# Kernel optimization log

Measured on AMD Instinct MI355X. Metric: run time of the kernel, lower is better.

Reference implementation:

```python
import jax, jax.numpy as jnp
import numpy as np

BITS = 4
GROUP_SIZE = 128
IN_FEATURES = 4096
OUT_FEATURES = 14336
M = 256  # rows of x; >= kernel_switch_threshold so torch takes the dequant+matmul path


def setup_inputs() -> dict:
    key = jax.random.key(0)
    k1, k2, k3, k4 = jax.random.split(key, 4)
    x = jax.random.normal(k1, (M, IN_FEATURES), dtype=jnp.float16)
    # packed int4 weights: in_features//32*bits rows of int32
    qweight = jax.random.randint(
        k2, (IN_FEATURES // 32 * BITS, OUT_FEATURES), 0, 2**31 - 1, dtype=jnp.int32
    )
    n_groups = IN_FEATURES // GROUP_SIZE
    scales = jax.random.uniform(k3, (n_groups, OUT_FEATURES), dtype=jnp.float32) * 0.01 + 0.001
    # note: module stores zeros as scale*zero product (see pack()); any float works
    zeros = jax.random.uniform(k4, (n_groups, OUT_FEATURES), dtype=jnp.float32) * 0.05
    return {"x": x, "qweight": qweight, "scales": scales, "zeros": zeros}


def reference(x, qweight, scales, zeros):
    # Unpack 8 int4 values from each int32 (little-endian nibbles), matching
    # torch: (qweight[:,None,:] >> wf) & 0xF with wf = [0,4,...,28].
    shifts = jnp.arange(0, 32, BITS, dtype=jnp.int32)          # [8]
    w = (qweight[:, None, :] >> shifts[None, :, None]) & (2**BITS - 1)  # [K/8, 8, N]
    w = w.reshape(-1, GROUP_SIZE, qweight.shape[1])             # [n_groups, group, N]
    s = scales.astype(jnp.float16)[:, None, :]                  # [n_groups, 1, N]
    z = zeros.astype(jnp.float16)[:, None, :]
    # group-wise asymmetric dequant: scale * q - (scale*zero)
    w = (s * w.astype(jnp.float16) - z).reshape(-1, qweight.shape[1])  # [K, N]
    out = jnp.matmul(x, w)                                      # [M, N] fp16
    return out.astype(x.dtype)
```

## Files before the change

### kernel.cpp

```cpp
#include <hip/hip_runtime.h>
#include <hip/hip_fp16.h>

typedef unsigned int u32;
typedef unsigned short u16;
typedef __attribute__((ext_vector_type(8))) _Float16 f16x8;
typedef __attribute__((ext_vector_type(4))) float f32x4;
typedef __attribute__((ext_vector_type(4))) u32 u32x4;

#define K_DIM 4096
#define N_DIM 14336
#define BM 64
#define BN 128
#define BK 64
#define NITER 32
#define NBLK 448
#define LDA 72

union U4F8 { u32x4 u; f16x8 v; };

__device__ __forceinline__ f16x8 dq8(u32 q, __half2 s2, __half2 d2, __half2 z2) {
  U4F8 r;
  const u32 x0 = ( q        & 0x000F000Fu) | 0x64006400u;
  const u32 x1 = ((q >> 4)  & 0x000F000Fu) | 0x64006400u;
  const u32 x2 = ((q >> 8)  & 0x000F000Fu) | 0x64006400u;
  const u32 x3 = ((q >> 12) & 0x000F000Fu) | 0x64006400u;
  r.u.x = __builtin_bit_cast(u32, __hsub2(__hfma2(__builtin_bit_cast(__half2, x0), s2, d2), z2));
  r.u.y = __builtin_bit_cast(u32, __hsub2(__hfma2(__builtin_bit_cast(__half2, x1), s2, d2), z2));
  r.u.z = __builtin_bit_cast(u32, __hsub2(__hfma2(__builtin_bit_cast(__half2, x2), s2, d2), z2));
  r.u.w = __builtin_bit_cast(u32, __hsub2(__hfma2(__builtin_bit_cast(__half2, x3), s2, d2), z2));
  return r.v;
}

__device__ __forceinline__ u32 pkrtz(float a, float b) {
  return __builtin_bit_cast(u32, __builtin_amdgcn_cvt_pkrtz(a, b));
}

__global__ __launch_bounds__(512, 4) void kivi_gemm(
    const float* __restrict__ X,
    const int* __restrict__ QW,
    const float* __restrict__ S,
    const float* __restrict__ Z,
    float* __restrict__ O)
{
  __shared__ __align__(16) u16 As[2][2][BM][LDA];

  const int tid  = threadIdx.x;
  const int lane = tid & 63;
  const int w    = tid >> 6;
  const int ws   = w >> 2;
  const int wl   = w & 3;
  const int stid = tid & 255;

  const int b  = blockIdx.x;
  const int L  = (b & 7) * 56 + (b >> 3);
  const int m0 = (L & 3) * BM;
  const int n0 = (L >> 2) * BN;

  const int wm = wl >> 1, wn = wl & 1;
  const int mb = wm * 32, nb = wn * 64;
  const int fr = lane & 15, fq = lane >> 4;
  const int cb = n0 + nb + fr;

  const int arow = stid >> 2;
  const int acol = (stid & 3) * 16;

  f32x4 acc[2][4];
#pragma unroll
  for (int mi = 0; mi < 2; ++mi)
#pragma unroll
    for (int ni = 0; ni < 4; ++ni)
      acc[mi][ni] = (f32x4){0.f, 0.f, 0.f, 0.f};

  f32x4 aReg[4];
  u32 qReg[2][4];
  float sv[4], zv[4];

  auto loadAx = [&](int t) {
    const float* p = X + (size_t)(m0 + arow) * K_DIM + t * BK + acol;
    aReg[0] = *(const f32x4*)(p);
    aReg[1] = *(const f32x4*)(p + 4);
    aReg[2] = *(const f32x4*)(p + 8);
    aReg[3] = *(const f32x4*)(p + 12);
  };
  auto writeAx = [&](int buf) {
#pragma unroll
    for (int c = 0; c < 2; ++c) {
      u32x4 pk;
      pk.x = pkrtz(aReg[c * 2][0], aReg[c * 2 + 1][0]);
      pk.y = pkrtz(aReg[c * 2][1], aReg[c * 2 + 1][1]);
      pk.z = pkrtz(aReg[c * 2][2], aReg[c * 2 + 1][2]);
      pk.w = pkrtz(aReg[c * 2][3], aReg[c * 2 + 1][3]);
      *(u32x4*)&As[ws][buf][arow][acol + c * 8] = pk;
    }
  };
  auto loadBq = [&](int t, int g) {
    const size_t rbase = (size_t)(t * 8 + fq) * N_DIM + cb;
#pragma unroll
    for (int ks = 0; ks < 2; ++ks)
#pragma unroll
      for (int ni = 0; ni < 4; ++ni)
        qReg[ks][ni] = *(const u32*)(QW + rbase + (size_t)ks * 4 * N_DIM + ni * 16);
#pragma unroll
    for (int ni = 0; ni < 4; ++ni) {
      sv[ni] = S[(size_t)g * N_DIM + cb + ni * 16];
      zv[ni] = Z[(size_t)g * N_DIM + cb + ni * 16];
    }
  };

  loadAx(ws);
  loadBq(ws, 0);
  writeAx(0);
  __syncthreads();

  const __half hneg1024 = __float2half(-1024.f);

  for (int i = 0; i < NITER; ++i) {
    const int t   = 2 * i + ws;
    const int cur = i & 1;
    const bool pf = (i + 1 < NITER);

    if (pf) loadAx(t + 2);

    __half2 s2[4], d2[4], z2[4];
#pragma unroll
    for (int ni = 0; ni < 4; ++ni) {
      const __half sh = __float2half(sv[ni]);
      const __half zh = __float2half(zv[ni]);
      const __half dh = __hmul(sh, hneg1024);
      s2[ni] = __halves2half2(sh, sh);
      d2[ni] = __halves2half2(dh, dh);
      z2[ni] = __halves2half2(zh, zh);
    }

#pragma unroll
    for (int ks = 0; ks < 2; ++ks) {
      f16x8 af[2], bf[4];
#pragma unroll
      for (int mi = 0; mi < 2; ++mi)
        af[mi] = *(const f16x8*)&As[ws][cur][mb + mi * 16 + fr][ks * 32 + fq * 8];
#pragma unroll
      for (int ni = 0; ni < 4; ++ni)
        bf[ni] = dq8(qReg[ks][ni], s2[ni], d2[ni], z2[ni]);
#pragma unroll
      for (int mi = 0; mi < 2; ++mi)
#pragma unroll
        for (int ni = 0; ni < 4; ++ni)
          acc[mi][ni] = __builtin_amdgcn_mfma_f32_16x16x32_f16(
              af[mi], bf[ni], acc[mi][ni], 0, 0, 0);
    }

    if (pf) {
      writeAx(cur ^ 1);
      loadBq(t + 2, i + 1);
    }
    __syncthreads();
  }

  float (*Lr)[132] = reinterpret_cast<float(*)[132]>(&As[0][0][0][0]);
  if (ws == 1) {
#pragma unroll
    for (int mi = 0; mi < 2; ++mi)
#pragma unroll
      for (int ni = 0; ni < 4; ++ni)
#pragma unroll
        for (int r = 0; r < 4; ++r)
          Lr[mb + mi * 16 + fq * 4 + r][nb + ni * 16 + fr] = acc[mi][ni][r];
  }
  __syncthreads();
  if (ws == 0) {
#pragma unroll
    for (int mi = 0; mi < 2; ++mi)
#pragma unroll
      for (int ni = 0; ni < 4; ++ni)
#pragma unroll
        for (int r = 0; r < 4; ++r) {
          const int row = mb + mi * 16 + fq * 4 + r;
          const int col = nb + ni * 16 + fr;
          O[(size_t)(m0 + row) * N_DIM + n0 + col] = acc[mi][ni][r] + Lr[row][col];
        }
  }
}

extern "C" void kernel_launch(void* const* d_in, const int* in_sizes, int n_in,
                              void* d_out, int out_size, void* d_ws, size_t ws_size,
                              hipStream_t stream) {
  const float* X  = (const float*)d_in[0];
  const int*   QW = (const int*)d_in[1];
  const float* S  = (const float*)d_in[2];
  const float* Zp = (const float*)d_in[3];
  float* O = (float*)d_out;
  hipLaunchKernelGGL(kivi_gemm, dim3(NBLK), dim3(512), 0, stream, X, QW, S, Zp, O);
}
```

Baseline: 76.78 us.

## Replace split-K warp groups with full-K 2x4 warp tiling and BK=128

Drops the two-way intra-block split-K (two warp sets on alternating K tiles with a final LDS reduction) and instead tiles all 8 warps as 2x4 over the 64x128 output, each warp covering 32x32 with full K. BK grows to 128, which matches the quantization group, so one scale/zero load per tile is needed, and the B weight loads are double-buffered in registers (current/next) and issued early alongside the A prefetch. This removes the LDS reduction epilogue and halves the per-warp dequant work per MFMA group. The cost is fewer MFMAs per A-fragment read and more register copies for the next-tile buffers.

```diff
diff --git a/kernel.cpp b/kernel.cpp
--- a/kernel.cpp
+++ b/kernel.cpp
@@ -11,19 +11,20 @@
 #define N_DIM 14336
 #define BM 64
 #define BN 128
-#define BK 64
-#define NITER 32
+#define BK 128
+#define NITER (K_DIM / BK)
 #define NBLK 448
-#define LDA 72
+#define LDA 136
 
 union U4F8 { u32x4 u; f16x8 v; };
 
 __device__ __forceinline__ f16x8 dq8(u32 q, __half2 s2, __half2 d2, __half2 z2) {
+  const u32 q1 = q >> 4, q2 = q >> 8, q3 = q >> 12;
   U4F8 r;
-  const u32 x0 = ( q        & 0x000F000Fu) | 0x64006400u;
-  const u32 x1 = ((q >> 4)  & 0x000F000Fu) | 0x64006400u;
-  const u32 x2 = ((q >> 8)  & 0x000F000Fu) | 0x64006400u;
-  const u32 x3 = ((q >> 12) & 0x000F000Fu) | 0x64006400u;
+  const u32 x0 = ( q & 0x000F000Fu) | 0x64006400u;
+  const u32 x1 = (q1 & 0x000F000Fu) | 0x64006400u;
+  const u32 x2 = (q2 & 0x000F000Fu) | 0x64006400u;
+  const u32 x3 = (q3 & 0x000F000Fu) | 0x64006400u;
   r.u.x = __builtin_bit_cast(u32, __hsub2(__hfma2(__builtin_bit_cast(__half2, x0), s2, d2), z2));
   r.u.y = __builtin_bit_cast(u32, __hsub2(__hfma2(__builtin_bit_cast(__half2, x1), s2, d2), z2));
   r.u.z = __builtin_bit_cast(u32, __hsub2(__hfma2(__builtin_bit_cast(__half2, x2), s2, d2), z2));
@@ -42,38 +43,35 @@
     const float* __restrict__ Z,
     float* __restrict__ O)
 {
-  __shared__ __align__(16) u16 As[2][2][BM][LDA];
+  __shared__ __align__(16) u16 As[2][BM][LDA];
 
   const int tid  = threadIdx.x;
   const int lane = tid & 63;
   const int w    = tid >> 6;
-  const int ws   = w >> 2;
-  const int wl   = w & 3;
-  const int stid = tid & 255;
 
   const int b  = blockIdx.x;
   const int L  = (b & 7) * 56 + (b >> 3);
   const int m0 = (L & 3) * BM;
   const int n0 = (L >> 2) * BN;
 
-  const int wm = wl >> 1, wn = wl & 1;
-  const int mb = wm * 32, nb = wn * 64;
+  const int wm = w >> 2, wn = w & 3;
+  const int mb = wm * 32, nb = wn * 32;
   const int fr = lane & 15, fq = lane >> 4;
   const int cb = n0 + nb + fr;
 
-  const int arow = stid >> 2;
-  const int acol = (stid & 3) * 16;
+  const int arow = tid >> 3;
+  const int acol = (tid & 7) * 16;
 
-  f32x4 acc[2][4];
+  f32x4 acc[2][2];
 #pragma unroll
   for (int mi = 0; mi < 2; ++mi)
 #pragma unroll
-    for (int ni = 0; ni < 4; ++ni)
+    for (int ni = 0; ni < 2; ++ni)
       acc[mi][ni] = (f32x4){0.f, 0.f, 0.f, 0.f};
 
   f32x4 aReg[4];
-  u32 qReg[2][4];
-  float sv[4], zv[4];
+  u32 qC[4][2], qN[4][2];
+  float svC[2], zvC[2], svN[2], zvN[2];
 
   auto loadAx = [&](int t) {
     const float* p = X + (size_t)(m0 + arow) * K_DIM + t * BK + acol;
@@ -90,42 +88,44 @@
       pk.y = pkrtz(aReg[c * 2][1], aReg[c * 2 + 1][1]);
       pk.z = pkrtz(aReg[c * 2][2], aReg[c * 2 + 1][2]);
       pk.w = pkrtz(aReg[c * 2][3], aReg[c * 2 + 1][3]);
-      *(u32x4*)&As[ws][buf][arow][acol + c * 8] = pk;
+      *(u32x4*)&As[buf][arow][acol + c * 8] = pk;
     }
   };
-  auto loadBq = [&](int t, int g) {
-    const size_t rbase = (size_t)(t * 8 + fq) * N_DIM + cb;
+  auto loadBq = [&](int t, u32 (&q)[4][2], float (&s)[2], float (&z)[2]) {
+    const size_t rbase = (size_t)(t * 16 + fq) * N_DIM + cb;
 #pragma unroll
-    for (int ks = 0; ks < 2; ++ks)
+    for (int ks = 0; ks < 4; ++ks)
 #pragma unroll
-      for (int ni = 0; ni < 4; ++ni)
-        qReg[ks][ni] = *(const u32*)(QW + rbase + (size_t)ks * 4 * N_DIM + ni * 16);
+      for (int ni = 0; ni < 2; ++ni)
+        q[ks][ni] = *(const u32*)(QW + rbase + (size_t)ks * 4 * N_DIM + ni * 16);
 #pragma unroll
-    for (int ni = 0; ni < 4; ++ni) {
-      sv[ni] = S[(size_t)g * N_DIM + cb + ni * 16];
-      zv[ni] = Z[(size_t)g * N_DIM + cb + ni * 16];
+    for (int ni = 0; ni < 2; ++ni) {
+      s[ni] = S[(size_t)t * N_DIM + cb + ni * 16];
+      z[ni] = Z[(size_t)t * N_DIM + cb + ni * 16];
     }
   };
 
-  loadAx(ws);
-  loadBq(ws, 0);
+  loadAx(0);
+  loadBq(0, qC, svC, zvC);
   writeAx(0);
   __syncthreads();
 
   const __half hneg1024 = __float2half(-1024.f);
 
   for (int i = 0; i < NITER; ++i) {
-    const int t   = 2 * i + ws;
     const int cur = i & 1;
     const bool pf = (i + 1 < NITER);
 
-    if (pf) loadAx(t + 2);
+    if (pf) {
+      loadAx(i + 1);
+      loadBq(i + 1, qN, svN, zvN);
+    }
 
-    __half2 s2[4], d2[4], z2[4];
+    __half2 s2[2], d2[2], z2[2];
 #pragma unroll
-    for (int ni = 0; ni < 4; ++ni) {
-      const __half sh = __float2half(sv[ni]);
-      const __half zh = __float2half(zv[ni]);
+    for (int ni = 0; ni < 2; ++ni) {
+      const __half sh = __float2half(svC[ni]);
+      const __half zh = __float2half(zvC[ni]);
       const __half dh = __hmul(sh, hneg1024);
       s2[ni] = __halves2half2(sh, sh);
       d2[ni] = __halves2half2(dh, dh);
@@ -133,52 +133,47 @@
     }
 
 #pragma unroll
-    for (int ks = 0; ks < 2; ++ks) {
-      f16x8 af[2], bf[4];
+    for (int ks = 0; ks < 4; ++ks) {
+      f16x8 af[2], bf[2];
 #pragma unroll
       for (int mi = 0; mi < 2; ++mi)
-        af[mi] = *(const f16x8*)&As[ws][cur][mb + mi * 16 + fr][ks * 32 + fq * 8];
+        af[mi] = *(const f16x8*)&As[cur][mb + mi * 16 + fr][ks * 32 + fq * 8];
 #pragma unroll
-      for (int ni = 0; ni < 4; ++ni)
-        bf[ni] = dq8(qReg[ks][ni], s2[ni], d2[ni], z2[ni]);
+      for (int ni = 0; ni < 2; ++ni)
+        bf[ni] = dq8(qC[ks][ni], s2[ni], d2[ni], z2[ni]);
 #pragma unroll
       for (int mi = 0; mi < 2; ++mi)
 #pragma unroll
-        for (int ni = 0; ni < 4; ++ni)
+        for (int ni = 0; ni < 2; ++ni)
           acc[mi][ni] = __builtin_amdgcn_mfma_f32_16x16x32_f16(
               af[mi], bf[ni], acc[mi][ni], 0, 0, 0);
     }
 
     if (pf) {
       writeAx(cur ^ 1);
-      loadBq(t + 2, i + 1);
+#pragma unroll
+      for (int ks = 0; ks < 4; ++ks)
+#pragma unroll
+        for (int ni = 0; ni < 2; ++ni)
+          qC[ks][ni] = qN[ks][ni];
+#pragma unroll
+      for (int ni = 0; ni < 2; ++ni) {
+        svC[ni] = svN[ni]; zvC[ni] = zvN[ni];
+      }
     }
     __syncthreads();
   }
 
-  float (*Lr)[132] = reinterpret_cast<float(*)[132]>(&As[0][0][0][0]);
-  if (ws == 1) {
 #pragma unroll
-    for (int mi = 0; mi < 2; ++mi)
+  for (int mi = 0; mi < 2; ++mi)
 #pragma unroll
-      for (int ni = 0; ni < 4; ++ni)
+    for (int ni = 0; ni < 2; ++ni)
 #pragma unroll
-        for (int r = 0; r < 4; ++r)
-          Lr[mb + mi * 16 + fq * 4 + r][nb + ni * 16 + fr] = acc[mi][ni][r];
-  }
-  __syncthreads();
-  if (ws == 0) {
-#pragma unroll
-    for (int mi = 0; mi < 2; ++mi)
-#pragma unroll
-      for (int ni = 0; ni < 4; ++ni)
-#pragma unroll
-        for (int r = 0; r < 4; ++r) {
-          const int row = mb + mi * 16 + fq * 4 + r;
-          const int col = nb + ni * 16 + fr;
-          O[(size_t)(m0 + row) * N_DIM + n0 + col] = acc[mi][ni][r] + Lr[row][col];
-        }
-  }
+      for (int r = 0; r < 4; ++r) {
+        const int row = m0 + mb + mi * 16 + fq * 4 + r;
+        const int col = n0 + nb + ni * 16 + fr;
+        O[(size_t)row * N_DIM + col] = acc[mi][ni][r];
+      }
 }
 
 extern "C" void kernel_launch(void* const* d_in, const int* in_sizes, int n_in,
```

New measurement: 77.73 us. About the same (+1.2%).
